# Kernel tuning notes

Measured on AMD Instinct MI355X. Metric: run time of the kernel, lower is better.

The kernel has to match this reference:

```python
import jax, jax.numpy as jnp
import numpy as np

NUM_TAGS = 64
BSZ = 256
SEQ_LEN = 2048


def setup_inputs() -> dict:
    key = jax.random.key(0)
    k1, k2, k3, k4, k5 = jax.random.split(key, 5)
    inputs = jax.random.normal(k1, (BSZ, SEQ_LEN, NUM_TAGS), dtype=jnp.float32)
    tags = jax.random.randint(k2, (BSZ, SEQ_LEN), 0, NUM_TAGS, dtype=jnp.int32)
    mask = jnp.ones((BSZ, SEQ_LEN), dtype=jnp.int32)
    # parameters (xavier-normal-ish transitions, normal start/end)
    std = float(np.sqrt(2.0 / (NUM_TAGS + NUM_TAGS)))
    transitions = jax.random.normal(k3, (NUM_TAGS, NUM_TAGS), dtype=jnp.float32) * std
    start_transitions = jax.random.normal(k4, (NUM_TAGS,), dtype=jnp.float32)
    end_transitions = jax.random.normal(k5, (NUM_TAGS,), dtype=jnp.float32)
    return {"inputs": inputs, "tags": tags, "mask": mask,
            "transitions": transitions,
            "start_transitions": start_transitions,
            "end_transitions": end_transitions}


def _input_likelihood(logits, maskf, transitions, start_transitions, end_transitions):
    # logits: (B, S, T); maskf: (B, S) float
    logits_t = jnp.transpose(logits, (1, 0, 2))   # (S, B, T)
    mask_t = maskf.T                               # (S, B)
    alpha0 = start_transitions[None, :] + logits_t[0]  # (B, T)

    def step(alpha, xs):
        emit, m = xs  # emit: (B, T), m: (B,)
        # inner[b, i, j] = alpha[b, i] + transitions[i, j] + emit[b, j]
        inner = alpha[:, :, None] + transitions[None, :, :] + emit[:, None, :]
        new_alpha = jax.nn.logsumexp(inner, axis=1)  # (B, T)
        alpha = new_alpha * m[:, None] + alpha * (1.0 - m[:, None])
        return alpha, None

    alpha, _ = jax.lax.scan(step, alpha0, (logits_t[1:], mask_t[1:]))
    stops = alpha + end_transitions[None, :]
    return jax.nn.logsumexp(stops, axis=-1)  # (B,)


def _joint_likelihood(logits, tags, mask, maskf, transitions, start_transitions, end_transitions):
    # logits: (B, S, T); tags, mask: (B, S)
    B = logits.shape[0]
    tags = tags * mask  # zero out padded positions
    score = start_transitions[tags[:, 0]]  # (B,)
    # transition scores for t -> t+1, masked by mask[t+1]
    trans = transitions[tags[:, :-1], tags[:, 1:]] * maskf[:, 1:]  # (B, S-1)
    # emission scores for t in [0, S-2], masked by mask[t]
    emit = jnp.take_along_axis(logits[:, :-1, :], tags[:, :-1, None], axis=2)[..., 0]
    emit = emit * maskf[:, :-1]  # (B, S-1)
    score = score + trans.sum(axis=1) + emit.sum(axis=1)
    # last valid tag
    last_idx = maskf.sum(axis=1).astype(jnp.int32) - 1  # (B,)
    batch_ar = jnp.arange(B)
    last_tags = tags[batch_ar, last_idx]  # (B,)
    last_transition_score = end_transitions[last_tags]
    last_input_score = logits[:, -1, :][batch_ar, last_tags]  # (B,)
    score = score + last_transition_score + last_input_score * maskf[:, -1]
    return score  # (B,)


def reference(inputs, tags, mask, transitions, start_transitions, end_transitions):
    maskf = mask.astype(jnp.float32)
    log_denominator = _input_likelihood(inputs, maskf, transitions,
                                        start_transitions, end_transitions)
    log_numerator = _joint_likelihood(inputs, tags, mask, maskf, transitions,
                                      start_transitions, end_transitions)
    return jnp.sum(log_numerator - log_denominator)
```

## Files before the change

kernel.cpp:

```cpp
#include <hip/hip_runtime.h>

#define BSZ 256
#define SEQ 2048
#define NT  64
#define KS  5.0f

#define CLT 8
#define SC  (16 * CLT)
#define NG  (SEQ / SC)

#define SROW  136
#define SSLAB (16 * SROW + 8)
#define RWS   68

typedef __fp16 half2_t __attribute__((ext_vector_type(2)));
typedef __fp16 half4_t __attribute__((ext_vector_type(4)));
typedef float  f32x4_t __attribute__((ext_vector_type(4)));
typedef int    int2_t  __attribute__((ext_vector_type(2)));

static __device__ __forceinline__ float wave_red_sum(float x) {
#pragma unroll
    for (int d = 1; d < 64; d <<= 1) x += __shfl_xor(x, d);
    return x;
}

static __device__ __forceinline__ half4_t pack4(float a, float b, float c, float d) {
    half2_t lo = __builtin_amdgcn_cvt_pkrtz(a, b);
    half2_t hi = __builtin_amdgcn_cvt_pkrtz(c, d);
    int2_t t;
    t.x = __builtin_bit_cast(int, lo);
    t.y = __builtin_bit_cast(int, hi);
    return __builtin_bit_cast(half4_t, t);
}

__global__ __launch_bounds__(128) void crf_pre_kernel(
    const float* __restrict__ trans,
    half4_t* __restrict__ EtabF,
    half4_t* __restrict__ EtabB)
{
    for (int e = threadIdx.x; e < 1024; e += 128) {
        int lane = e & 63, slot = e >> 6;
        int q = slot >> 2, kc = slot & 3;
        int rlo = lane & 15, h = lane >> 4;
        int m = 16 * q + rlo;
        float f[4], bb[4];
#pragma unroll
        for (int i = 0; i < 4; ++i) {
            int k = 16 * kc + 4 * h + i;
            f[i]  = __expf(trans[k * NT + m]);
            bb[i] = __expf(trans[m * NT + k]);
        }
        EtabF[e] = pack4(f[0], f[1], f[2], f[3]);
        EtabB[e] = pack4(bb[0], bb[1], bb[2], bb[3]);
    }
}

__global__ __launch_bounds__(128) void crf_fat_kernel(
    const float* __restrict__ logits,
    const int*   __restrict__ tags,
    const int*   __restrict__ mask,
    const float* __restrict__ trans,
    const float* __restrict__ startT,
    const float* __restrict__ endT,
    const half4_t* __restrict__ EtabF,
    const half4_t* __restrict__ EtabB,
    float* __restrict__ rB,
    float* __restrict__ wB,
    float* __restrict__ Jpart,
    float* __restrict__ numtrans)
{
    __shared__ __align__(16) unsigned char Flds[CLT * SSLAB];
    __shared__ int   lmbits[16];
    __shared__ float jred[2];

    if (blockIdx.x < BSZ) {
        const int b   = blockIdx.x;
        const int tid = threadIdx.x;
        float* redf = (float*)Flds;
        int*   redi = (int*)(Flds + 512);

        const int*   __restrict__ tg = tags + (size_t)b * SEQ;
        const int*   __restrict__ mk = mask + (size_t)b * SEQ;
        const float* __restrict__ Lr = logits + (size_t)b * SEQ * NT;

        float acc = 0.0f;
        int   cnt = 0;
        for (int t = tid; t < SEQ; t += 128) {
            int mt  = mk[t];
            cnt += mt;
            int tgt = tg[t] * mt;
            if (t < SEQ - 1) {
                int m1 = mk[t + 1];
                acc += trans[tgt * NT + tg[t + 1] * m1] * (float)m1;
                acc += Lr[t * NT + tgt] * (float)mt;
            }
        }
        redf[tid] = acc;
        redi[tid] = cnt;
        __syncthreads();
        for (int off = 64; off > 0; off >>= 1) {
            if (tid < off) {
                redf[tid] += redf[tid + off];
                redi[tid] += redi[tid + off];
            }
            __syncthreads();
        }
        if (tid == 0) {
            int   last_idx = redi[0] - 1;
            int   m_last   = mk[SEQ - 1];
            int   tag0     = tg[0] * mk[0];
            int   last_tag = tg[last_idx] * mk[last_idx];
            float r = redf[0] + startT[tag0] + endT[last_tag];
            r += Lr[(size_t)(SEQ - 1) * NT + last_tag] * (float)m_last;
            numtrans[b] = r;
        }
        return;
    }

    const int blk  = blockIdx.x - BSZ;
    const int b    = blk / NG;
    const int g    = blk % NG;
    const int tid  = threadIdx.x;
    const bool fwd = (tid >> 6) == 0;
    const int lane = tid & 63;
    const int rlo  = lane & 15;
    const int h    = lane >> 4;

    const float* __restrict__ Lg = logits + ((size_t)b * SEQ + (size_t)g * SC) * NT;
#pragma unroll
    for (int hh = 0; hh < 2; ++hh) {
        f32x4_t xb[8];
#pragma unroll
        for (int jj = 0; jj < 8; ++jj) {
            int gci = (hh * 8 + jj) * 128 + tid;
            xb[jj] = *(const f32x4_t*)(Lg + (size_t)(gci >> 4) * NT + (gci & 15) * 4);
        }
#pragma unroll
        for (int jj = 0; jj < 8; ++jj) {
            int gci = (hh * 8 + jj) * 128 + tid;
            int row = gci >> 4;
            int col = gci & 15;
            int k   = row / CLT;
            int s   = row % CLT;
            half2_t p0 = __builtin_amdgcn_cvt_pkrtz(__expf(xb[jj][0] - KS), __expf(xb[jj][1] - KS));
            half2_t p1 = __builtin_amdgcn_cvt_pkrtz(__expf(xb[jj][2] - KS), __expf(xb[jj][3] - KS));
            int2_t w;
            w.x = __builtin_bit_cast(int, p0);
            w.y = __builtin_bit_cast(int, p1);
            *(int2_t*)(Flds + s * SSLAB + k * SROW + col * 8) = w;
        }
    }
    if (tid < 16) {
        const int* mk = mask + (size_t)b * SEQ + (size_t)g * SC + tid * CLT;
        int bits = 0;
#pragma unroll
        for (int s = 0; s < CLT; ++s) bits |= (mk[s] ? 1 : 0) << s;
        if (g == 0 && tid == 0) bits &= ~1;
        lmbits[tid] = bits;
    }

    const half4_t* __restrict__ Et = fwd ? EtabF : EtabB;
    half4_t A[4][4];
#pragma unroll
    for (int q = 0; q < 4; ++q)
#pragma unroll
        for (int kc = 0; kc < 4; ++kc)
            A[q][kc] = Et[(q * 4 + kc) * 64 + lane];

    __syncthreads();

    const int mbits = lmbits[rlo];
    f32x4_t V[4];
    float C = 0.0f;
#pragma unroll
    for (int q = 0; q < 4; ++q)
#pragma unroll
        for (int i = 0; i < 4; ++i) V[q][i] = 1.0f;

    if (fwd && g == 0 && rlo == 0) {
        float mx = -1e30f;
        f32x4_t al[4];
#pragma unroll
        for (int q = 0; q < 4; ++q) {
            f32x4_t em = *(const f32x4_t*)(logits + (size_t)b * SEQ * NT + 16 * q + 4 * h);
            f32x4_t st = *(const f32x4_t*)(startT + 16 * q + 4 * h);
#pragma unroll
            for (int i = 0; i < 4; ++i) {
                al[q][i] = st[i] + em[i];
                mx = fmaxf(mx, al[q][i]);
            }
        }
        mx = fmaxf(mx, __shfl_xor(mx, 16));
        mx = fmaxf(mx, __shfl_xor(mx, 32));
        C = mx;
#pragma unroll
        for (int q = 0; q < 4; ++q)
#pragma unroll
            for (int i = 0; i < 4; ++i) V[q][i] = __expf(al[q][i] - mx);
    }

    const unsigned char* Fbase = Flds + rlo * SROW + h * 8;

    if (fwd) {
#pragma unroll
        for (int s = 0; s < CLT; ++s) {
            half4_t Fh[4];
#pragma unroll
            for (int q = 0; q < 4; ++q)
                Fh[q] = *(const half4_t*)(Fbase + s * SSLAB + q * 32);
            half4_t Xh[4];
#pragma unroll
            for (int kc = 0; kc < 4; ++kc)
                Xh[kc] = pack4(V[kc][0], V[kc][1], V[kc][2], V[kc][3]);
            f32x4_t Y[4];
#pragma unroll
            for (int q = 0; q < 4; ++q) {
                f32x4_t a0 = {0.0f, 0.0f, 0.0f, 0.0f};
                f32x4_t a1 = {0.0f, 0.0f, 0.0f, 0.0f};
                a0 = __builtin_amdgcn_mfma_f32_16x16x16f16(A[q][0], Xh[0], a0, 0, 0, 0);
                a0 = __builtin_amdgcn_mfma_f32_16x16x16f16(A[q][1], Xh[1], a0, 0, 0, 0);
                a1 = __builtin_amdgcn_mfma_f32_16x16x16f16(A[q][2], Xh[2], a1, 0, 0, 0);
                a1 = __builtin_amdgcn_mfma_f32_16x16x16f16(A[q][3], Xh[3], a1, 0, 0, 0);
                Y[q] = a0 + a1;
            }
            int mt = (mbits >> s) & 1;
#pragma unroll
            for (int q = 0; q < 4; ++q)
#pragma unroll
                for (int i = 0; i < 4; ++i) {
                    float w = Y[q][i] * (float)Fh[q][i];
                    V[q][i] = mt ? w : V[q][i];
                }
            C += mt ? KS : 0.0f;
        }
        {
            float mx = V[0][0];
#pragma unroll
            for (int q = 0; q < 4; ++q)
#pragma unroll
                for (int i = 0; i < 4; ++i) mx = fmaxf(mx, V[q][i]);
            mx = fmaxf(mx, __shfl_xor(mx, 16));
            mx = fmaxf(mx, __shfl_xor(mx, 32));
            mx = fmaxf(mx, 1e-30f);
            float inv = 1.0f / mx;
#pragma unroll
            for (int q = 0; q < 4; ++q)
#pragma unroll
                for (int i = 0; i < 4; ++i) V[q][i] *= inv;
            C += __logf(mx);
        }
    } else {
#pragma unroll
        for (int s = CLT - 1; s >= 0; --s) {
            half4_t Fh[4];
#pragma unroll
            for (int kc = 0; kc < 4; ++kc)
                Fh[kc] = *(const half4_t*)(Fbase + s * SSLAB + kc * 32);
            half4_t Xh[4];
#pragma unroll
            for (int kc = 0; kc < 4; ++kc)
                Xh[kc] = pack4(V[kc][0] * (float)Fh[kc][0],
                               V[kc][1] * (float)Fh[kc][1],
                               V[kc][2] * (float)Fh[kc][2],
                               V[kc][3] * (float)Fh[kc][3]);
            f32x4_t Y[4];
#pragma unroll
            for (int q = 0; q < 4; ++q) {
                f32x4_t a0 = {0.0f, 0.0f, 0.0f, 0.0f};
                f32x4_t a1 = {0.0f, 0.0f, 0.0f, 0.0f};
                a0 = __builtin_amdgcn_mfma_f32_16x16x16f16(A[q][0], Xh[0], a0, 0, 0, 0);
                a0 = __builtin_amdgcn_mfma_f32_16x16x16f16(A[q][1], Xh[1], a0, 0, 0, 0);
                a1 = __builtin_amdgcn_mfma_f32_16x16x16f16(A[q][2], Xh[2], a1, 0, 0, 0);
                a1 = __builtin_amdgcn_mfma_f32_16x16x16f16(A[q][3], Xh[3], a1, 0, 0, 0);
                Y[q] = a0 + a1;
            }
            int mt = (mbits >> s) & 1;
#pragma unroll
            for (int q = 0; q < 4; ++q)
#pragma unroll
                for (int i = 0; i < 4; ++i)
                    V[q][i] = mt ? Y[q][i] : V[q][i];
        }
    }

    __syncthreads();
    float* Rarr = (float*)Flds;
    float* Warr = Rarr + 16 * RWS;
    {
        float* dst = (fwd ? Rarr : Warr) + rlo * RWS + 4 * h;
#pragma unroll
        for (int q = 0; q < 4; ++q) *(f32x4_t*)(dst + 16 * q) = V[q];
    }
    __syncthreads();

    float part = 0.0f;
    {
        int c0 = fwd ? 1 : 9;
        int c1 = fwd ? 8 : 15;
        for (int c = c0; c <= c1; ++c) {
            float rv = Rarr[(c - 1) * RWS + lane];
            float wv = Warr[c * RWS + lane];
            float dot = wave_red_sum(rv * wv);
            float rho = wave_red_sum(wv);
            part += __logf(dot) - __logf(rho);
        }
        if (fwd) part += wave_red_sum((h == 0) ? C : 0.0f);
    }
    if (lane == 0) jred[fwd ? 0 : 1] = part;
    __syncthreads();
    if (tid == 0) Jpart[b * NG + g] = jred[0] + jred[1];

    if (fwd && rlo == 15) {
        float* dst = rB + ((size_t)b * NG + g) * 64 + 4 * h;
#pragma unroll
        for (int q = 0; q < 4; ++q) *(f32x4_t*)(dst + 16 * q) = V[q];
    }
    if (!fwd && rlo == 0) {
        float* dst = wB + ((size_t)b * NG + g) * 64 + 4 * h;
#pragma unroll
        for (int q = 0; q < 4; ++q) *(f32x4_t*)(dst + 16 * q) = V[q];
    }
}

__global__ __launch_bounds__(64) void crf_glue_kernel(
    const float* __restrict__ rB,
    const float* __restrict__ wB,
    const float* __restrict__ Jpart,
    const float* __restrict__ endT,
    float* __restrict__ den)
{
    const int b = blockIdx.x;
    const int j = threadIdx.x;

    float acc = (j < NG) ? Jpart[b * NG + j] : 0.0f;
    acc = wave_red_sum(acc);

    float part = 0.0f;
    for (int g = 1; g < NG; ++g) {
        float rv = rB[((size_t)b * NG + g - 1) * 64 + j];
        float wv = wB[((size_t)b * NG + g) * 64 + j];
        float dot = wave_red_sum(rv * wv);
        float rho = wave_red_sum(wv);
        part += __logf(dot) - __logf(rho);
    }
    float fin = wave_red_sum(rB[((size_t)b * NG + NG - 1) * 64 + j] * __expf(endT[j]));

    if (j == 0) den[b] = acc + part + __logf(fin);
}

__global__ __launch_bounds__(256) void crf_reduce_kernel(
    const float* __restrict__ den,
    const float* __restrict__ numtrans,
    float* __restrict__ out)
{
    __shared__ float red[256];
    const int tid = threadIdx.x;
    red[tid] = numtrans[tid] - den[tid];
    __syncthreads();
    for (int off = 128; off > 0; off >>= 1) {
        if (tid < off) red[tid] += red[tid + off];
        __syncthreads();
    }
    if (tid == 0) out[0] = red[0];
}

extern "C" void kernel_launch(void* const* d_in, const int* in_sizes, int n_in,
                              void* d_out, int out_size, void* d_ws, size_t ws_size,
                              hipStream_t stream)
{
    const float* logits = (const float*)d_in[0];
    const int*   tags   = (const int*)  d_in[1];
    const int*   mask   = (const int*)  d_in[2];
    const float* trans  = (const float*)d_in[3];
    const float* startT = (const float*)d_in[4];
    const float* endT   = (const float*)d_in[5];
    float* out = (float*)d_out;
    float* ws  = (float*)d_ws;

    float*   den      = ws;
    float*   numtrans = ws + BSZ;
    float*   Jpart    = ws + 2 * BSZ;
    float*   rB       = Jpart + (size_t)BSZ * NG;
    float*   wB       = rB + (size_t)BSZ * NG * 64;
    half4_t* EtabF    = (half4_t*)(wB + (size_t)BSZ * NG * 64);
    half4_t* EtabB    = EtabF + 1024;

    crf_pre_kernel<<<1, 128, 0, stream>>>(trans, EtabF, EtabB);
    crf_fat_kernel<<<BSZ + BSZ * NG, 128, 0, stream>>>(
        logits, tags, mask, trans, startT, endT, EtabF, EtabB, rB, wB, Jpart, numtrans);
    crf_glue_kernel<<<BSZ, 64, 0, stream>>>(rB, wB, Jpart, endT, den);
    crf_reduce_kernel<<<1, 256, 0, stream>>>(den, numtrans, out);
}
```

Before: 62.56 us.

## Drop forward renormalization and restructure per-chunk junction reduction with DPP

The forward pass no longer renormalizes V by its max at the end of the chunk. The constant KS contribution is now computed up front with popcount instead of being accumulated per step. The junction log-ratio computation is rewritten so that a single forward wave computes all 16 dot/sum pairs in parallel: each group of 4 lanes handles one chunk boundary, combines partials with DPP xor shuffles, and then does one wave reduction. This replaces 16 sequential double reductions split across two waves, and removes a shared-memory exchange and a __syncthreads. Skipping the renormalization risks overflow or precision loss if values grow across the chunk.

New measurement: 57.89 us. -7.5%, faster.

```diff
diff --git a/kernel.cpp b/kernel.cpp
--- a/kernel.cpp
+++ b/kernel.cpp
@@ -22,6 +22,15 @@
 #pragma unroll
     for (int d = 1; d < 64; d <<= 1) x += __shfl_xor(x, d);
     return x;
+}
+
+static __device__ __forceinline__ float dpp_xor1(float v) {
+    return __builtin_bit_cast(float,
+        __builtin_amdgcn_update_dpp(0, __builtin_bit_cast(int, v), 0xB1, 0xF, 0xF, true));
+}
+static __device__ __forceinline__ float dpp_xor2(float v) {
+    return __builtin_bit_cast(float,
+        __builtin_amdgcn_update_dpp(0, __builtin_bit_cast(int, v), 0x4E, 0xF, 0xF, true));
 }
 
 static __device__ __forceinline__ half4_t pack4(float a, float b, float c, float d) {
@@ -70,8 +79,7 @@
     float* __restrict__ numtrans)
 {
     __shared__ __align__(16) unsigned char Flds[CLT * SSLAB];
-    __shared__ int   lmbits[16];
-    __shared__ float jred[2];
+    __shared__ int lmbits[16];
 
     if (blockIdx.x < BSZ) {
         const int b   = blockIdx.x;
@@ -171,7 +179,7 @@
 
     const int mbits = lmbits[rlo];
     f32x4_t V[4];
-    float C = 0.0f;
+    float C = KS * (float)__builtin_popcount(mbits);
 #pragma unroll
     for (int q = 0; q < 4; ++q)
 #pragma unroll
@@ -192,7 +200,7 @@
         }
         mx = fmaxf(mx, __shfl_xor(mx, 16));
         mx = fmaxf(mx, __shfl_xor(mx, 32));
-        C = mx;
+        C += mx;
 #pragma unroll
         for (int q = 0; q < 4; ++q)
 #pragma unroll
@@ -231,23 +239,6 @@
                     float w = Y[q][i] * (float)Fh[q][i];
                     V[q][i] = mt ? w : V[q][i];
                 }
-            C += mt ? KS : 0.0f;
-        }
-        {
-            float mx = V[0][0];
-#pragma unroll
-            for (int q = 0; q < 4; ++q)
-#pragma unroll
-                for (int i = 0; i < 4; ++i) mx = fmaxf(mx, V[q][i]);
-            mx = fmaxf(mx, __shfl_xor(mx, 16));
-            mx = fmaxf(mx, __shfl_xor(mx, 32));
-            mx = fmaxf(mx, 1e-30f);
-            float inv = 1.0f / mx;
-#pragma unroll
-            for (int q = 0; q < 4; ++q)
-#pragma unroll
-                for (int i = 0; i < 4; ++i) V[q][i] *= inv;
-            C += __logf(mx);
         }
     } else {
 #pragma unroll
@@ -293,32 +284,44 @@
     }
     __syncthreads();
 
-    float part = 0.0f;
-    {
-        int c0 = fwd ? 1 : 9;
-        int c1 = fwd ? 8 : 15;
-        for (int c = c0; c <= c1; ++c) {
-            float rv = Rarr[(c - 1) * RWS + lane];
-            float wv = Warr[c * RWS + lane];
-            float dot = wave_red_sum(rv * wv);
-            float rho = wave_red_sum(wv);
-            part += __logf(dot) - __logf(rho);
-        }
-        if (fwd) part += wave_red_sum((h == 0) ? C : 0.0f);
-    }
-    if (lane == 0) jred[fwd ? 0 : 1] = part;
-    __syncthreads();
-    if (tid == 0) Jpart[b * NG + g] = jred[0] + jred[1];
-
-    if (fwd && rlo == 15) {
-        float* dst = rB + ((size_t)b * NG + g) * 64 + 4 * h;
-#pragma unroll
-        for (int q = 0; q < 4; ++q) *(f32x4_t*)(dst + 16 * q) = V[q];
-    }
-    if (!fwd && rlo == 0) {
-        float* dst = wB + ((size_t)b * NG + g) * 64 + 4 * h;
-#pragma unroll
-        for (int q = 0; q < 4; ++q) *(f32x4_t*)(dst + 16 * q) = V[q];
+    if (fwd) {
+        const int c   = lane >> 2;
+        const int sub = lane & 3;
+        float dot = 0.0f, rho = 0.0f;
+        {
+            const float* br = Rarr + (c == 0 ? 0 : (c - 1)) * RWS + sub * 16;
+            const float* bw = Warr + c * RWS + sub * 16;
+#pragma unroll
+            for (int u = 0; u < 4; ++u) {
+                f32x4_t rv = *(const f32x4_t*)(br + 4 * u);
+                f32x4_t wv = *(const f32x4_t*)(bw + 4 * u);
+#pragma unroll
+                for (int i = 0; i < 4; ++i) {
+                    dot = fmaf(rv[i], wv[i], dot);
+                    rho += wv[i];
+                }
+            }
+        }
+        dot += dpp_xor1(dot); dot += dpp_xor2(dot);
+        rho += dpp_xor1(rho); rho += dpp_xor2(rho);
+
+        float part = 0.0f;
+        if (c >= 1 && sub == 0) part = __logf(dot) - __logf(rho);
+        if (h == 0) part += C;
+        float tot = wave_red_sum(part);
+        if (lane == 0) Jpart[b * NG + g] = tot;
+
+        if (rlo == 15) {
+            float* dst = rB + ((size_t)b * NG + g) * 64 + 4 * h;
+#pragma unroll
+            for (int q = 0; q < 4; ++q) *(f32x4_t*)(dst + 16 * q) = V[q];
+        }
+    } else {
+        if (rlo == 0) {
+            float* dst = wB + ((size_t)b * NG + g) * 64 + 4 * h;
+#pragma unroll
+            for (int q = 0; q < 4; ++q) *(f32x4_t*)(dst + 16 * q) = V[q];
+        }
     }
 }
 
```
